# Optimization experiments

Measured on AMD Instinct MI355X. Metric: run time of the kernel, lower is better.

Reference implementation:

```python
import jax, jax.numpy as jnp
import numpy as np

NUM_HEADS = 12

def setup_inputs() -> dict:
    key = jax.random.key(0)
    k1, k2, k3 = jax.random.split(key, 3)
    B, T, S, C = 8, 40, 1024, 768
    N = T + S
    x = jax.random.normal(k1, (B, N, C), dtype=jnp.float32)
    qkv_w = jax.random.normal(k2, (3 * C, C), dtype=jnp.float32) * (C ** -0.5)
    proj_w = jax.random.normal(k3, (C, C), dtype=jnp.float32) * (C ** -0.5)
    proj_b = jnp.zeros((C,), dtype=jnp.float32)
    return {"x": x, "qkv_w": qkv_w, "proj_w": proj_w, "proj_b": proj_b,
            "image_tokens": S, "text_tokens": T}


def reference(x, qkv_w, proj_w, proj_b, image_tokens, text_tokens):
    B, N, C = x.shape
    H = NUM_HEADS
    hd = C // H
    scale = hd ** -0.5
    # qkv: [B,N,3C] -> [3,B,H,N,hd]
    qkv = jnp.einsum('bnc,dc->bnd', x, qkv_w)
    qkv = qkv.reshape(B, N, 3, H, hd).transpose(2, 0, 3, 1, 4)
    q, k, v = qkv[0], qkv[1], qkv[2]
    # text block comes first in the token axis
    q_mt, q_s = q[:, :, :text_tokens], q[:, :, text_tokens:]
    k_mt = k[:, :, :text_tokens]
    v_mt = v[:, :, :text_tokens]
    # text -> text attention
    attn_mt = jax.nn.softmax(jnp.einsum('bhtd,bhsd->bhts', q_mt, k_mt) * scale, axis=-1)
    x_mt = jnp.einsum('bhts,bhsd->bhtd', attn_mt, v_mt)
    x_mt = x_mt.transpose(0, 2, 1, 3).reshape(B, text_tokens, C)
    # image -> all attention
    attn_s = jax.nn.softmax(jnp.einsum('bhid,bhnd->bhin', q_s, k) * scale, axis=-1)
    x_s = jnp.einsum('bhin,bhnd->bhid', attn_s, v)
    x_s = x_s.transpose(0, 2, 1, 3).reshape(B, image_tokens, C)
    out = jnp.concatenate([x_mt, x_s], axis=1)
    out = jnp.einsum('bnc,dc->bnd', out, proj_w) + proj_b
    return out
```

## Files before the change

kernel.cpp:

```cpp
#include <hip/hip_runtime.h>
#include <hip/hip_bf16.h>

typedef __bf16 bf16x8 __attribute__((ext_vector_type(8)));
typedef float f32x4 __attribute__((ext_vector_type(4)));

#define NHEADS 12
#define TT 40
#define ST 1024
#define NTOK 1064
#define CDIM 768
#define HD 64

union U4 {
    uint4 u;
    __hip_bfloat16 h[8];
    bf16x8 v;
};

__device__ __forceinline__ void load_lds16(const __hip_bfloat16* g, __hip_bfloat16* s)
{
    __builtin_amdgcn_global_load_lds(
        (const __attribute__((address_space(1))) void*)g,
        (__attribute__((address_space(3))) void*)s, 16, 0, 0);
}

__global__ __launch_bounds__(256) void f2b3(
    const float* __restrict__ x,  __hip_bfloat16* __restrict__ xo,
    const float* __restrict__ w,  __hip_bfloat16* __restrict__ wo,
    const float* __restrict__ p,  __hip_bfloat16* __restrict__ po)
{
    const float* in; __hip_bfloat16* out; int i;
    if (blockIdx.x < 3192)      { in = x; out = xo; i = blockIdx.x * 256 + threadIdx.x; if (i >= 817152) return; }
    else if (blockIdx.x < 4056) { in = w; out = wo; i = (blockIdx.x - 3192) * 256 + threadIdx.x; if (i >= 221184) return; }
    else                        { in = p; out = po; i = (blockIdx.x - 4056) * 256 + threadIdx.x; if (i >= 73728) return; }
    float4 a = ((const float4*)in)[2 * i];
    float4 b = ((const float4*)in)[2 * i + 1];
    U4 r;
    r.h[0] = __float2bfloat16(a.x); r.h[1] = __float2bfloat16(a.y);
    r.h[2] = __float2bfloat16(a.z); r.h[3] = __float2bfloat16(a.w);
    r.h[4] = __float2bfloat16(b.x); r.h[5] = __float2bfloat16(b.y);
    r.h[6] = __float2bfloat16(b.z); r.h[7] = __float2bfloat16(b.w);
    ((uint4*)out)[i] = r.u;
}

template <int MODE>
__global__ __launch_bounds__(256) void gemm128(
    const __hip_bfloat16* __restrict__ A, int lda, int M,
    const __hip_bfloat16* __restrict__ B, int ldb,
    int K,
    __hip_bfloat16* __restrict__ out0,
    __hip_bfloat16* __restrict__ out1,
    __hip_bfloat16* __restrict__ out2,
    float* __restrict__ outf,
    const float* __restrict__ biasf)
{
    __shared__ __hip_bfloat16 lds[8704];
    __hip_bfloat16* ldsA = lds;
    __hip_bfloat16* ldsB = lds + 128 * 32;

    const int tid = threadIdx.x;
    const int m0 = blockIdx.y * 128;
    const int n0 = blockIdx.x * 128;
    const int w = tid >> 6, l = tid & 63, l15 = l & 15, lq = l >> 4;
    const int wm = w >> 1, wn = w & 1;

    const __hip_bfloat16* srcA[2];
    const __hip_bfloat16* srcB[2];
#pragma unroll
    for (int rd = 0; rd < 2; ++rd) {
        const int c = tid + rd * 256;
        const int r = c >> 2, cs = c & 3;
        const int gs = (cs - (r >> 1)) & 3;
        int ra = m0 + r; if (ra > M - 1) ra = M - 1;
        srcA[rd] = A + (long long)ra * lda + gs * 8;
        srcB[rd] = B + (long long)(n0 + r) * ldb + gs * 8;
    }

    int offA[4], offB[4];
#pragma unroll
    for (int t = 0; t < 4; ++t) {
        { const int r = wm * 64 + t * 16 + l15;
          offA[t] = r * 32 + ((lq + (r >> 1)) & 3) * 8; }
        { const int r = wn * 64 + t * 16 + l15;
          offB[t] = r * 32 + ((lq + (r >> 1)) & 3) * 8; }
    }

    f32x4 acc[4][4] = {};

    const int ksteps = K / 32;
    for (int ks = 0; ks < ksteps; ++ks) {
        __syncthreads();
#pragma unroll
        for (int rd = 0; rd < 2; ++rd) {
            const int c8 = (tid + rd * 256) * 8;
            load_lds16(srcA[rd] + ks * 32, ldsA + c8);
            load_lds16(srcB[rd] + ks * 32, ldsB + c8);
        }
        __syncthreads();

        bf16x8 af[4], bfr[4];
#pragma unroll
        for (int t = 0; t < 4; ++t) af[t] = *(const bf16x8*)(ldsA + offA[t]);
#pragma unroll
        for (int t = 0; t < 4; ++t) bfr[t] = *(const bf16x8*)(ldsB + offB[t]);
#pragma unroll
        for (int tr = 0; tr < 4; ++tr)
#pragma unroll
            for (int tc = 0; tc < 4; ++tc)
                acc[tr][tc] = __builtin_amdgcn_mfma_f32_16x16x32_bf16(af[tr], bfr[tc], acc[tr][tc], 0, 0, 0);
    }

    if (MODE == 0 && n0 >= 1536) {
        __hip_bfloat16* ldsT = lds;
#pragma unroll
        for (int hf = 0; hf < 2; ++hf) {
            __syncthreads();
            if (wn == hf) {
#pragma unroll
                for (int tr = 0; tr < 4; ++tr)
#pragma unroll
                    for (int tc = 0; tc < 4; ++tc) {
                        const int cl = tc * 16 + l15;
                        const int r = wm * 64 + tr * 16 + lq * 4;
                        U4 pk4;
                        pk4.h[0] = __float2bfloat16(acc[tr][tc][0]);
                        pk4.h[1] = __float2bfloat16(acc[tr][tc][1]);
                        pk4.h[2] = __float2bfloat16(acc[tr][tc][2]);
                        pk4.h[3] = __float2bfloat16(acc[tr][tc][3]);
                        *(uint2*)(ldsT + cl * 136 + r) = make_uint2(pk4.u.x, pk4.u.y);
                    }
            }
            __syncthreads();
            const int e = tid >> 2, rseg = (tid & 3) * 32;
            const int hh = (n0 + hf * 64 - 1536) >> 6;
#pragma unroll
            for (int j4 = 0; j4 < 4; ++j4) {
                const int r = rseg + j4 * 8;
                const int row = m0 + r;
                if (row >= 8 * NTOK) continue;
                const int b = row / NTOK;
                const int n = row - b * NTOK;
                __hip_bfloat16* dst = out2 + (((long long)(b * NHEADS + hh)) * HD + e) * NTOK + n;
                if (n + 8 <= NTOK) {
                    *(uint4*)dst = *(const uint4*)(ldsT + e * 136 + r);
                } else {
                    for (int j = 0; j < 8; ++j) {
                        const int row2 = row + j;
                        const int b2 = row2 / NTOK;
                        const int n2 = row2 - b2 * NTOK;
                        out2[(((long long)(b2 * NHEADS + hh)) * HD + e) * NTOK + n2] = ldsT[e * 136 + r + j];
                    }
                }
            }
        }
    } else {
#pragma unroll
        for (int tr = 0; tr < 4; ++tr) {
#pragma unroll
            for (int tc = 0; tc < 4; ++tc) {
                const int col = n0 + wn * 64 + tc * 16 + l15;
#pragma unroll
                for (int i = 0; i < 4; ++i) {
                    const int row = m0 + wm * 64 + tr * 16 + lq * 4 + i;
                    if (row >= M) continue;
                    const float v = acc[tr][tc][i];
                    if (MODE == 0) {
                        const int b = row / NTOK;
                        const int n = row - b * NTOK;
                        const int tq = col / CDIM;
                        const int rem = col - tq * CDIM;
                        const int h = rem >> 6;
                        const int e = rem & 63;
                        const long long gh = (long long)b * NHEADS + h;
                        const __hip_bfloat16 hv = __float2bfloat16(v);
                        if (tq == 0) out0[(gh * NTOK + n) * HD + e] = hv;
                        else         out1[(gh * NTOK + n) * HD + e] = hv;
                    } else {
                        outf[(long long)row * CDIM + col] = v + biasf[col];
                    }
                }
            }
        }
    }
}

__global__ __launch_bounds__(256) void flash_img(
    const __hip_bfloat16* __restrict__ Q,
    const __hip_bfloat16* __restrict__ Kt,
    const __hip_bfloat16* __restrict__ VT,
    __hip_bfloat16* __restrict__ AO)
{
    __shared__ __hip_bfloat16 smem[16384];
    const int gh = blockIdx.x;
    const int qt = blockIdx.y;
    const int tid = threadIdx.x;
    const int w = tid >> 6, l = tid & 63, l15 = l & 15, lq = l >> 4;

    const __hip_bfloat16* Qg = Q + ((long long)gh * NTOK + TT + qt * 128) * HD;
    const __hip_bfloat16* Kg = Kt + (long long)gh * NTOK * HD;
    const __hip_bfloat16* Vg = VT + (long long)gh * HD * NTOK;

    const int c0 = tid, c1 = tid + 256;
    const int r0 = c0 >> 3, r1 = c1 >> 3;
    const int g0 = ((c0 & 7) - r0) & 7;
    const int g1 = ((c1 & 7) - r1) & 7;

    bf16x8 qf[2][2];
#pragma unroll
    for (int s = 0; s < 2; ++s)
#pragma unroll
        for (int kk = 0; kk < 2; ++kk)
            qf[s][kk] = *(const bf16x8*)(Qg + (w * 32 + s * 16 + l15) * HD + kk * 32 + lq * 8);

    f32x4 ot[4][2] = {};
    float lrow[2] = {0.0f, 0.0f};

    load_lds16(Kg + (long long)r0 * HD + g0 * 8, smem + c0 * 8);
    load_lds16(Kg + (long long)r1 * HD + g1 * 8, smem + c1 * 8);
    load_lds16(Vg + (long long)r0 * NTOK + g0 * 8, smem + 4096 + c0 * 8);
    load_lds16(Vg + (long long)r1 * NTOK + g1 * 8, smem + 4096 + c1 * 8);

    const int segA = ((lq + l15) & 7) * 8;
    const int segB = ((4 + lq + l15) & 7) * 8;

    for (int kt = 0; kt < 17; ++kt) {
        __syncthreads();

        if (kt < 16) {
            const int np = (kt + 1) * 64;
            __hip_bfloat16* kb = smem + ((kt + 1) & 1) * 8192;
            __hip_bfloat16* vb = kb + 4096;
            int kr0 = np + r0; if (kr0 > NTOK - 1) kr0 = NTOK - 1;
            int kr1 = np + r1; if (kr1 > NTOK - 1) kr1 = NTOK - 1;
            load_lds16(Kg + (long long)kr0 * HD + g0 * 8, kb + c0 * 8);
            load_lds16(Kg + (long long)kr1 * HD + g1 * 8, kb + c1 * 8);
            int vc0 = np + g0 * 8; if (vc0 > NTOK - 8) vc0 = NTOK - 8;
            int vc1 = np + g1 * 8; if (vc1 > NTOK - 8) vc1 = NTOK - 8;
            load_lds16(Vg + (long long)r0 * NTOK + vc0, vb + c0 * 8);
            load_lds16(Vg + (long long)r1 * NTOK + vc1, vb + c1 * 8);
        }

        const __hip_bfloat16* kbuf = smem + (kt & 1) * 8192;
        const __hip_bfloat16* vbuf = kbuf + 4096;

        f32x4 st[4][2] = {};
#pragma unroll
        for (int kk = 0; kk < 2; ++kk) {
            const int seg = kk ? segB : segA;
            bf16x8 kf[4];
#pragma unroll
            for (int t = 0; t < 4; ++t)
                kf[t] = *(const bf16x8*)(kbuf + (t * 16 + l15) * 64 + seg);
#pragma unroll
            for (int t = 0; t < 4; ++t)
#pragma unroll
                for (int s = 0; s < 2; ++s)
                    st[t][s] = __builtin_amdgcn_mfma_f32_16x16x32_bf16(kf[t], qf[s][kk], st[t][s], 0, 0, 0);
        }

        if (kt == 16) {
#pragma unroll
            for (int t = 0; t < 4; ++t) {
                const int nb = 1024 + t * 16 + lq * 4;
#pragma unroll
                for (int i = 0; i < 4; ++i)
                    if (nb + i >= NTOK) { st[t][0][i] = -1e30f; st[t][1][i] = -1e30f; }
            }
        }

#pragma unroll
        for (int s = 0; s < 2; ++s) {
            float rs = 0.0f;
#pragma unroll
            for (int t = 0; t < 4; ++t)
#pragma unroll
                for (int i = 0; i < 4; ++i) {
                    const float p = exp2f(st[t][s][i] * 0.18033688f);
                    st[t][s][i] = p;
                    rs += p;
                }
            lrow[s] += rs;
        }

        unsigned pk[4][2][2];
#pragma unroll
        for (int t = 0; t < 4; ++t)
#pragma unroll
            for (int s = 0; s < 2; ++s)
#pragma unroll
                for (int h = 0; h < 2; ++h) {
                    __hip_bfloat162 b2 = __float22bfloat162_rn(
                        make_float2(st[t][s][2 * h], st[t][s][2 * h + 1]));
                    pk[t][s][h] = *(unsigned*)&b2;
                }

        const int L0 = ((l & 16) ? 32 : 0) + l15;
        const int L1 = L0 + 16;
        const bool hi = (l & 32) != 0;
#pragma unroll
        for (int kk = 0; kk < 2; ++kk) {
            const int seg = kk ? segB : segA;
            bf16x8 vf[4];
#pragma unroll
            for (int te = 0; te < 4; ++te)
                vf[te] = *(const bf16x8*)(vbuf + (te * 16 + l15) * 64 + seg);
#pragma unroll
            for (int s = 0; s < 2; ++s) {
                const unsigned a0 = __shfl(pk[2 * kk][s][0], L0), b0 = __shfl(pk[2 * kk + 1][s][0], L0);
                const unsigned a1 = __shfl(pk[2 * kk][s][1], L0), b1 = __shfl(pk[2 * kk + 1][s][1], L0);
                const unsigned a2 = __shfl(pk[2 * kk][s][0], L1), b2 = __shfl(pk[2 * kk + 1][s][0], L1);
                const unsigned a3 = __shfl(pk[2 * kk][s][1], L1), b3 = __shfl(pk[2 * kk + 1][s][1], L1);
                union { unsigned u[4]; bf16x8 v; } pu;
                pu.u[0] = hi ? b0 : a0;
                pu.u[1] = hi ? b1 : a1;
                pu.u[2] = hi ? b2 : a2;
                pu.u[3] = hi ? b3 : a3;
#pragma unroll
                for (int te = 0; te < 4; ++te)
                    ot[te][s] = __builtin_amdgcn_mfma_f32_16x16x32_bf16(vf[te], pu.v, ot[te][s], 0, 0, 0);
            }
        }
    }

#pragma unroll
    for (int s = 0; s < 2; ++s) {
        lrow[s] += __shfl_xor(lrow[s], 16);
        lrow[s] += __shfl_xor(lrow[s], 32);
    }

    __syncthreads();
    __hip_bfloat16* obuf = smem;
    const float inv[2] = {1.0f / lrow[0], 1.0f / lrow[1]};
#pragma unroll
    for (int te = 0; te < 4; ++te)
#pragma unroll
        for (int s = 0; s < 2; ++s) {
            __hip_bfloat162 x0, x1;
            x0.x = __float2bfloat16(ot[te][s][0] * inv[s]);
            x0.y = __float2bfloat16(ot[te][s][1] * inv[s]);
            x1.x = __float2bfloat16(ot[te][s][2] * inv[s]);
            x1.y = __float2bfloat16(ot[te][s][3] * inv[s]);
            uint2 u;
            u.x = *(unsigned*)&x0;
            u.y = *(unsigned*)&x1;
            *(uint2*)(obuf + (w * 32 + s * 16 + l15) * 72 + te * 16 + lq * 4) = u;
        }
    __syncthreads();
    {
        const int b = gh / NHEADS, h = gh - b * NHEADS;
        const int r = tid >> 1, cc = (tid & 1) * 32;
        const int token = TT + qt * 128 + r;
        __hip_bfloat16* dst = AO + ((long long)b * NTOK + token) * CDIM + h * HD + cc;
#pragma unroll
        for (int i = 0; i < 4; ++i)
            *(uint4*)(dst + i * 8) = *(const uint4*)(obuf + r * 72 + cc + i * 8);
    }
}

__global__ __launch_bounds__(256) void text_attn(
    const __hip_bfloat16* __restrict__ Q,
    const __hip_bfloat16* __restrict__ Kt,
    const __hip_bfloat16* __restrict__ VT,
    __hip_bfloat16* __restrict__ AO)
{
    const int gh = blockIdx.x;
    const int b = gh / NHEADS;
    const int h = gh - b * NHEADS;
    __shared__ float smem[3 * 40 * 65];
    float* Qs = smem;
    float* Ks = smem + 40 * 65;
    float* Vs = smem + 2 * 40 * 65;
    const __hip_bfloat16* Qg = Q + (long long)gh * NTOK * HD;
    const __hip_bfloat16* Kg = Kt + (long long)gh * NTOK * HD;
    const __hip_bfloat16* Vg = VT + (long long)gh * HD * NTOK;
    for (int idx = threadIdx.x; idx < 40 * 64; idx += 256) {
        const int n = idx >> 6;
        const int e = idx & 63;
        Qs[n * 65 + e] = __bfloat162float(Qg[n * HD + e]);
        Ks[n * 65 + e] = __bfloat162float(Kg[n * HD + e]);
        Vs[n * 65 + e] = __bfloat162float(Vg[(long long)e * NTOK + n]);
    }
    __syncthreads();
    const int w = threadIdx.x >> 6;
    const int lane = threadIdx.x & 63;
    for (int i = w; i < TT; i += 4) {
        float s = -1e30f;
        if (lane < TT) {
            float a = 0.0f;
            for (int e = 0; e < 64; ++e) a += Qs[i * 65 + e] * Ks[lane * 65 + e];
            s = a * 0.125f;
        }
        float m = s;
        for (int off = 32; off > 0; off >>= 1) m = fmaxf(m, __shfl_xor(m, off));
        float pr = (lane < TT) ? __expf(s - m) : 0.0f;
        float ssum = pr;
        for (int off = 32; off > 0; off >>= 1) ssum += __shfl_xor(ssum, off);
        pr /= ssum;
        float o = 0.0f;
        for (int j = 0; j < TT; ++j) o += __shfl(pr, j) * Vs[j * 65 + lane];
        AO[((long long)b * NTOK + i) * CDIM + h * HD + lane] = __float2bfloat16(o);
    }
}

extern "C" void kernel_launch(void* const* d_in, const int* in_sizes, int n_in,
                              void* d_out, int out_size, void* d_ws, size_t ws_size,
                              hipStream_t stream)
{
    const float* x      = (const float*)d_in[0];
    const float* qkv_w  = (const float*)d_in[1];
    const float* proj_w = (const float*)d_in[2];
    const float* proj_b = (const float*)d_in[3];
    float* out = (float*)d_out;

    const long long QKV_ELEMS = (long long)8 * NHEADS * NTOK * HD;
    __hip_bfloat16* Q  = (__hip_bfloat16*)d_ws;
    __hip_bfloat16* Kt = Q + QKV_ELEMS;
    __hip_bfloat16* VT = Kt + QKV_ELEMS;
    __hip_bfloat16* AO = VT + QKV_ELEMS;
    __hip_bfloat16* xb = AO;
    __hip_bfloat16* wb = AO + QKV_ELEMS;
    __hip_bfloat16* pb = wb + (long long)3 * CDIM * CDIM;

    f2b3<<<4344, 256, 0, stream>>>(x, xb, qkv_w, wb, proj_w, pb);

    gemm128<0><<<dim3(18, 67), 256, 0, stream>>>(
        xb, CDIM, 8 * NTOK, wb, CDIM, CDIM,
        Q, Kt, VT, nullptr, nullptr);

    text_attn<<<96, 256, 0, stream>>>(Q, Kt, VT, AO);

    flash_img<<<dim3(96, 8), 256, 0, stream>>>(Q, Kt, VT, AO);

    gemm128<3><<<dim3(6, 67), 256, 0, stream>>>(
        AO, CDIM, 8 * NTOK, pb, CDIM, CDIM,
        nullptr, nullptr, nullptr, out, proj_b);
}
```

Before: 255.6 us.

## Split image attention across 8 waves and fold softmax scale into Q

The image flash-attention kernel now runs 512 threads per block, with each wave handling 16 query rows instead of 32. This halves per-thread accumulator and score registers, which should improve occupancy and latency hiding. The softmax scale times log2(e) is folded into Q during the QKV GEMM epilogue, which removes a multiply per score in both attention kernels. The cost is that every wave reads K and V fragments from LDS for fewer rows, so LDS traffic per unit of compute doubles.

```diff
diff --git a/kernel.cpp b/kernel.cpp
--- a/kernel.cpp
+++ b/kernel.cpp
@@ -10,6 +10,7 @@
 #define NTOK 1064
 #define CDIM 768
 #define HD 64
+#define QSCALE 0.18033688f
 
 union U4 {
     uint4 u;
@@ -172,9 +173,8 @@
                         const int h = rem >> 6;
                         const int e = rem & 63;
                         const long long gh = (long long)b * NHEADS + h;
-                        const __hip_bfloat16 hv = __float2bfloat16(v);
-                        if (tq == 0) out0[(gh * NTOK + n) * HD + e] = hv;
-                        else         out1[(gh * NTOK + n) * HD + e] = hv;
+                        if (tq == 0) out0[(gh * NTOK + n) * HD + e] = __float2bfloat16(v * QSCALE);
+                        else         out1[(gh * NTOK + n) * HD + e] = __float2bfloat16(v);
                     } else {
                         outf[(long long)row * CDIM + col] = v + biasf[col];
                     }
@@ -184,7 +184,7 @@
     }
 }
 
-__global__ __launch_bounds__(256) void flash_img(
+__global__ __launch_bounds__(512) void flash_img(
     const __hip_bfloat16* __restrict__ Q,
     const __hip_bfloat16* __restrict__ Kt,
     const __hip_bfloat16* __restrict__ VT,
@@ -200,28 +200,25 @@
     const __hip_bfloat16* Kg = Kt + (long long)gh * NTOK * HD;
     const __hip_bfloat16* Vg = VT + (long long)gh * HD * NTOK;
 
-    const int c0 = tid, c1 = tid + 256;
-    const int r0 = c0 >> 3, r1 = c1 >> 3;
-    const int g0 = ((c0 & 7) - r0) & 7;
-    const int g1 = ((c1 & 7) - r1) & 7;
-
-    bf16x8 qf[2][2];
-#pragma unroll
-    for (int s = 0; s < 2; ++s)
-#pragma unroll
-        for (int kk = 0; kk < 2; ++kk)
-            qf[s][kk] = *(const bf16x8*)(Qg + (w * 32 + s * 16 + l15) * HD + kk * 32 + lq * 8);
-
-    f32x4 ot[4][2] = {};
-    float lrow[2] = {0.0f, 0.0f};
-
-    load_lds16(Kg + (long long)r0 * HD + g0 * 8, smem + c0 * 8);
-    load_lds16(Kg + (long long)r1 * HD + g1 * 8, smem + c1 * 8);
-    load_lds16(Vg + (long long)r0 * NTOK + g0 * 8, smem + 4096 + c0 * 8);
-    load_lds16(Vg + (long long)r1 * NTOK + g1 * 8, smem + 4096 + c1 * 8);
+    const int r0 = tid >> 3;
+    const int g0 = ((tid & 7) - r0) & 7;
+
+    bf16x8 qf[2];
+#pragma unroll
+    for (int kk = 0; kk < 2; ++kk)
+        qf[kk] = *(const bf16x8*)(Qg + (w * 16 + l15) * HD + kk * 32 + lq * 8);
+
+    f32x4 ot[4] = {};
+    float lsum = 0.0f;
+
+    load_lds16(Kg + (long long)r0 * HD + g0 * 8, smem + tid * 8);
+    load_lds16(Vg + (long long)r0 * NTOK + g0 * 8, smem + 4096 + tid * 8);
 
     const int segA = ((lq + l15) & 7) * 8;
     const int segB = ((4 + lq + l15) & 7) * 8;
+    const int L0 = ((l & 16) ? 32 : 0) + l15;
+    const int L1 = L0 + 16;
+    const bool hi = (l & 32) != 0;
 
     for (int kt = 0; kt < 17; ++kt) {
         __syncthreads();
@@ -229,21 +226,16 @@
         if (kt < 16) {
             const int np = (kt + 1) * 64;
             __hip_bfloat16* kb = smem + ((kt + 1) & 1) * 8192;
-            __hip_bfloat16* vb = kb + 4096;
-            int kr0 = np + r0; if (kr0 > NTOK - 1) kr0 = NTOK - 1;
-            int kr1 = np + r1; if (kr1 > NTOK - 1) kr1 = NTOK - 1;
-            load_lds16(Kg + (long long)kr0 * HD + g0 * 8, kb + c0 * 8);
-            load_lds16(Kg + (long long)kr1 * HD + g1 * 8, kb + c1 * 8);
-            int vc0 = np + g0 * 8; if (vc0 > NTOK - 8) vc0 = NTOK - 8;
-            int vc1 = np + g1 * 8; if (vc1 > NTOK - 8) vc1 = NTOK - 8;
-            load_lds16(Vg + (long long)r0 * NTOK + vc0, vb + c0 * 8);
-            load_lds16(Vg + (long long)r1 * NTOK + vc1, vb + c1 * 8);
+            int kr = np + r0; if (kr > NTOK - 1) kr = NTOK - 1;
+            int vc = np + g0 * 8; if (vc > NTOK - 8) vc = NTOK - 8;
+            load_lds16(Kg + (long long)kr * HD + g0 * 8, kb + tid * 8);
+            load_lds16(Vg + (long long)r0 * NTOK + vc, kb + 4096 + tid * 8);
         }
 
         const __hip_bfloat16* kbuf = smem + (kt & 1) * 8192;
         const __hip_bfloat16* vbuf = kbuf + 4096;
 
-        f32x4 st[4][2] = {};
+        f32x4 st[4] = {};
 #pragma unroll
         for (int kk = 0; kk < 2; ++kk) {
             const int seg = kk ? segB : segA;
@@ -253,9 +245,7 @@
                 kf[t] = *(const bf16x8*)(kbuf + (t * 16 + l15) * 64 + seg);
 #pragma unroll
             for (int t = 0; t < 4; ++t)
-#pragma unroll
-                for (int s = 0; s < 2; ++s)
-                    st[t][s] = __builtin_amdgcn_mfma_f32_16x16x32_bf16(kf[t], qf[s][kk], st[t][s], 0, 0, 0);
+                st[t] = __builtin_amdgcn_mfma_f32_16x16x32_bf16(kf[t], qf[kk], st[t], 0, 0, 0);
         }
 
         if (kt == 16) {
@@ -264,39 +254,31 @@
                 const int nb = 1024 + t * 16 + lq * 4;
 #pragma unroll
                 for (int i = 0; i < 4; ++i)
-                    if (nb + i >= NTOK) { st[t][0][i] = -1e30f; st[t][1][i] = -1e30f; }
-            }
-        }
-
-#pragma unroll
-        for (int s = 0; s < 2; ++s) {
-            float rs = 0.0f;
-#pragma unroll
-            for (int t = 0; t < 4; ++t)
-#pragma unroll
-                for (int i = 0; i < 4; ++i) {
-                    const float p = exp2f(st[t][s][i] * 0.18033688f);
-                    st[t][s][i] = p;
-                    rs += p;
-                }
-            lrow[s] += rs;
-        }
-
-        unsigned pk[4][2][2];
+                    if (nb + i >= NTOK) st[t][i] = -1e30f;
+            }
+        }
+
+        float rs = 0.0f;
 #pragma unroll
         for (int t = 0; t < 4; ++t)
 #pragma unroll
-            for (int s = 0; s < 2; ++s)
-#pragma unroll
-                for (int h = 0; h < 2; ++h) {
-                    __hip_bfloat162 b2 = __float22bfloat162_rn(
-                        make_float2(st[t][s][2 * h], st[t][s][2 * h + 1]));
-                    pk[t][s][h] = *(unsigned*)&b2;
-                }
-
-        const int L0 = ((l & 16) ? 32 : 0) + l15;
-        const int L1 = L0 + 16;
-        const bool hi = (l & 32) != 0;
+            for (int i = 0; i < 4; ++i) {
+                const float p = exp2f(st[t][i]);
+                st[t][i] = p;
+                rs += p;
+            }
+        lsum += rs;
+
+        unsigned pk[4][2];
+#pragma unroll
+        for (int t = 0; t < 4; ++t)
+#pragma unroll
+            for (int h = 0; h < 2; ++h) {
+                __hip_bfloat162 b2 = __float22bfloat162_rn(
+                    make_float2(st[t][2 * h], st[t][2 * h + 1]));
+                pk[t][h] = *(unsigned*)&b2;
+            }
+
 #pragma unroll
         for (int kk = 0; kk < 2; ++kk) {
             const int seg = kk ? segB : segA;
@@ -304,56 +286,47 @@
 #pragma unroll
             for (int te = 0; te < 4; ++te)
                 vf[te] = *(const bf16x8*)(vbuf + (te * 16 + l15) * 64 + seg);
-#pragma unroll
-            for (int s = 0; s < 2; ++s) {
-                const unsigned a0 = __shfl(pk[2 * kk][s][0], L0), b0 = __shfl(pk[2 * kk + 1][s][0], L0);
-                const unsigned a1 = __shfl(pk[2 * kk][s][1], L0), b1 = __shfl(pk[2 * kk + 1][s][1], L0);
-                const unsigned a2 = __shfl(pk[2 * kk][s][0], L1), b2 = __shfl(pk[2 * kk + 1][s][0], L1);
-                const unsigned a3 = __shfl(pk[2 * kk][s][1], L1), b3 = __shfl(pk[2 * kk + 1][s][1], L1);
-                union { unsigned u[4]; bf16x8 v; } pu;
-                pu.u[0] = hi ? b0 : a0;
-                pu.u[1] = hi ? b1 : a1;
-                pu.u[2] = hi ? b2 : a2;
-                pu.u[3] = hi ? b3 : a3;
-#pragma unroll
-                for (int te = 0; te < 4; ++te)
-                    ot[te][s] = __builtin_amdgcn_mfma_f32_16x16x32_bf16(vf[te], pu.v, ot[te][s], 0, 0, 0);
-            }
-        }
-    }
-
-#pragma unroll
-    for (int s = 0; s < 2; ++s) {
-        lrow[s] += __shfl_xor(lrow[s], 16);
-        lrow[s] += __shfl_xor(lrow[s], 32);
-    }
+            const unsigned a0 = __shfl(pk[2 * kk][0], L0), b0 = __shfl(pk[2 * kk + 1][0], L0);
+            const unsigned a1 = __shfl(pk[2 * kk][1], L0), b1 = __shfl(pk[2 * kk + 1][1], L0);
+            const unsigned a2 = __shfl(pk[2 * kk][0], L1), b2 = __shfl(pk[2 * kk + 1][0], L1);
+            const unsigned a3 = __shfl(pk[2 * kk][1], L1), b3 = __shfl(pk[2 * kk + 1][1], L1);
+            union { unsigned u[4]; bf16x8 v; } pu;
+            pu.u[0] = hi ? b0 : a0;
+            pu.u[1] = hi ? b1 : a1;
+            pu.u[2] = hi ? b2 : a2;
+            pu.u[3] = hi ? b3 : a3;
+#pragma unroll
+            for (int te = 0; te < 4; ++te)
+                ot[te] = __builtin_amdgcn_mfma_f32_16x16x32_bf16(vf[te], pu.v, ot[te], 0, 0, 0);
+        }
+    }
+
+    lsum += __shfl_xor(lsum, 16);
+    lsum += __shfl_xor(lsum, 32);
 
     __syncthreads();
     __hip_bfloat16* obuf = smem;
-    const float inv[2] = {1.0f / lrow[0], 1.0f / lrow[1]};
-#pragma unroll
-    for (int te = 0; te < 4; ++te)
-#pragma unroll
-        for (int s = 0; s < 2; ++s) {
-            __hip_bfloat162 x0, x1;
-            x0.x = __float2bfloat16(ot[te][s][0] * inv[s]);
-            x0.y = __float2bfloat16(ot[te][s][1] * inv[s]);
-            x1.x = __float2bfloat16(ot[te][s][2] * inv[s]);
-            x1.y = __float2bfloat16(ot[te][s][3] * inv[s]);
-            uint2 u;
-            u.x = *(unsigned*)&x0;
-            u.y = *(unsigned*)&x1;
-            *(uint2*)(obuf + (w * 32 + s * 16 + l15) * 72 + te * 16 + lq * 4) = u;
-        }
+    const float inv = 1.0f / lsum;
+#pragma unroll
+    for (int te = 0; te < 4; ++te) {
+        __hip_bfloat162 x0, x1;
+        x0.x = __float2bfloat16(ot[te][0] * inv);
+        x0.y = __float2bfloat16(ot[te][1] * inv);
+        x1.x = __float2bfloat16(ot[te][2] * inv);
+        x1.y = __float2bfloat16(ot[te][3] * inv);
+        uint2 u;
+        u.x = *(unsigned*)&x0;
+        u.y = *(unsigned*)&x1;
+        *(uint2*)(obuf + (w * 16 + l15) * 72 + te * 16 + lq * 4) = u;
+    }
     __syncthreads();
     {
         const int b = gh / NHEADS, h = gh - b * NHEADS;
-        const int r = tid >> 1, cc = (tid & 1) * 32;
+        const int r = tid >> 2, cc = (tid & 3) * 16;
         const int token = TT + qt * 128 + r;
         __hip_bfloat16* dst = AO + ((long long)b * NTOK + token) * CDIM + h * HD + cc;
-#pragma unroll
-        for (int i = 0; i < 4; ++i)
-            *(uint4*)(dst + i * 8) = *(const uint4*)(obuf + r * 72 + cc + i * 8);
+        *(uint4*)dst       = *(const uint4*)(obuf + r * 72 + cc);
+        *(uint4*)(dst + 8) = *(const uint4*)(obuf + r * 72 + cc + 8);
     }
 }
 
@@ -388,11 +361,11 @@
         if (lane < TT) {
             float a = 0.0f;
             for (int e = 0; e < 64; ++e) a += Qs[i * 65 + e] * Ks[lane * 65 + e];
-            s = a * 0.125f;
+            s = a;
         }
         float m = s;
         for (int off = 32; off > 0; off >>= 1) m = fmaxf(m, __shfl_xor(m, off));
-        float pr = (lane < TT) ? __expf(s - m) : 0.0f;
+        float pr = (lane < TT) ? exp2f(s - m) : 0.0f;
         float ssum = pr;
         for (int off = 32; off > 0; off >>= 1) ssum += __shfl_xor(ssum, off);
         pr /= ssum;
@@ -429,7 +402,7 @@
 
     text_attn<<<96, 256, 0, stream>>>(Q, Kt, VT, AO);
 
-    flash_img<<<dim3(96, 8), 256, 0, stream>>>(Q, Kt, VT, AO);
+    flash_img<<<dim3(96, 8), 512, 0, stream>>>(Q, Kt, VT, AO);
 
     gemm128<3><<<dim3(6, 67), 256, 0, stream>>>(
         AO, CDIM, 8 * NTOK, pb, CDIM, CDIM,
```

Result: faster. 244.9 us (-4.2%).
